# Performance work log

Measured on AMD Instinct MI355X. Metric: run time of the kernel, lower is better.

Reference implementation:

```python
import jax, jax.numpy as jnp
import numpy as np

EMBED_DIM = 768
N_HEADS = 12
HEAD_SIZE = EMBED_DIM // N_HEADS
SCALE = HEAD_SIZE ** -0.5


def setup_inputs() -> dict:
    key = jax.random.key(0)
    k1, k2, k3, k4, k5 = jax.random.split(key, 5)
    B, T, C = 2, 4096, EMBED_DIM
    x = jax.random.normal(k1, (B, T, C), dtype=jnp.float32)
    # nn.Linear(embed_dim, 3*embed_dim): weight [3C, C], bias [3C]
    w_attn = jax.random.normal(k2, (3 * C, C), dtype=jnp.float32) * (C ** -0.5)
    b_attn = jax.random.normal(k3, (3 * C,), dtype=jnp.float32) * 0.02
    # nn.Linear(embed_dim, embed_dim)
    w_proj = jax.random.normal(k4, (C, C), dtype=jnp.float32) * (C ** -0.5)
    b_proj = jax.random.normal(k5, (C,), dtype=jnp.float32) * 0.02
    return {"x": x, "w_attn": w_attn, "b_attn": b_attn, "w_proj": w_proj, "b_proj": b_proj}


def reference(x, w_attn, b_attn, w_proj, b_proj):
    b, t, c = x.shape
    qkv = jnp.einsum('btc,dc->btd', x, w_attn) + b_attn  # [b,t,3c]
    q, k, v = jnp.split(qkv, 3, axis=-1)
    # [b, h, t, hs]
    q = q.reshape(b, t, N_HEADS, HEAD_SIZE).transpose(0, 2, 1, 3)
    k = k.reshape(b, t, N_HEADS, HEAD_SIZE).transpose(0, 2, 1, 3)
    v = v.reshape(b, t, N_HEADS, HEAD_SIZE).transpose(0, 2, 1, 3)
    scores = jnp.einsum('bhqd,bhkd->bhqk', q, k) * SCALE  # [b,h,t,t]
    causal = jnp.tril(jnp.ones((t, t), dtype=bool))
    scores = jnp.where(causal[None, None], scores, -jnp.inf)
    attn = jax.nn.softmax(scores, axis=-1)
    out = jnp.einsum('bhqk,bhkd->bhqd', attn, v)  # [b,h,t,hs]
    out = out.transpose(0, 2, 1, 3).reshape(b, t, c)
    out = jnp.einsum('btc,dc->btd', out, w_proj) + b_proj
    return out
```

## Files before the change

kernel.cpp:

```cpp
#include <hip/hip_runtime.h>
#include <hip/hip_bf16.h>

#define T_SEQ 4096
#define C_EMB 768
#define NH_ 12
#define HS_ 64
#define B_SZ 2
#define M_TOK 8192
#define N_QKV 2304

typedef __attribute__((ext_vector_type(8))) __bf16 bf16x8;
typedef __attribute__((ext_vector_type(8))) unsigned short ushort8v;
typedef __attribute__((ext_vector_type(2))) unsigned int uint2v;
typedef __attribute__((ext_vector_type(4))) unsigned int uint4v;
typedef __attribute__((ext_vector_type(4))) float f32x4;

__device__ __forceinline__ unsigned short f2bf(float f) {
  __hip_bfloat16 h = __float2bfloat16(f);
  return __builtin_bit_cast(unsigned short, h);
}

__device__ __forceinline__ unsigned int cvtpk(float lo, float hi) {
  unsigned int r;
  asm("v_cvt_pk_bf16_f32 %0, %1, %2" : "=v"(r) : "v"(lo), "v"(hi));
  return r;
}

__device__ __forceinline__ float fast_exp2(float x) {
  float r;
  asm("v_exp_f32 %0, %1" : "=v"(r) : "v"(x));
  return r;
}

#define GLOAD_LDS16(gp, lp)                                                   \
  __builtin_amdgcn_global_load_lds(                                           \
      (const __attribute__((address_space(1))) void*)(gp),                    \
      (__attribute__((address_space(3))) void*)(lp), 16, 0, 0)

#define KSWZ(row, bytecol) ((((row) * 128) + ((bytecol) ^ (((row) & 7) << 4))))

#define LOG2E 1.4426950408889634f

#define CVT_N0 (M_TOK * C_EMB)
#define CVT_N1 (N_QKV * C_EMB)
#define CVT_N2 (C_EMB * C_EMB)
__global__ void cvt_all_bf16(const float* __restrict__ x,
                             const float* __restrict__ wa,
                             const float* __restrict__ wp,
                             unsigned short* __restrict__ out) {
  int i = (blockIdx.x * 256 + threadIdx.x) * 8;
  const float* src;
  int j;
  if (i < CVT_N0) { src = x; j = i; }
  else if (i < CVT_N0 + CVT_N1) { src = wa; j = i - CVT_N0; }
  else { src = wp; j = i - CVT_N0 - CVT_N1; }
  float4 a = *reinterpret_cast<const float4*>(&src[j]);
  float4 b = *reinterpret_cast<const float4*>(&src[j + 4]);
  uint4v o;
  o.x = cvtpk(a.x, a.y);
  o.y = cvtpk(a.z, a.w);
  o.z = cvtpk(b.x, b.y);
  o.w = cvtpk(b.z, b.w);
  *reinterpret_cast<uint4v*>(&out[i]) = o;
}

template <int MODE, int BM, int BN>
__global__ __launch_bounds__(256) void gemm_bt_kernel(
    const unsigned short* __restrict__ A, const unsigned short* __restrict__ Bw,
    const float* __restrict__ bias, unsigned short* __restrict__ qo,
    unsigned short* __restrict__ ko, unsigned short* __restrict__ vo,
    float* __restrict__ fo, int Kdim, int Ndim) {
  constexpr int MF = BM / 32;
  constexpr int NF = BN / 32;
  __shared__ __align__(16) char as_[BM * 128];
  __shared__ __align__(16) char bs_[BN * 128];
  const int tid = threadIdx.x;
  const int lane = tid & 63;
  const int wid = tid >> 6;
  const int g = lane >> 4;
  const int l15 = lane & 15;
  const int m0 = blockIdx.y * BM;
  const int n0 = blockIdx.x * BN;
  const int wm = (wid >> 1) * (BM / 2);
  const int wn = (wid & 1) * (BN / 2);

  const int lrow = lane >> 3;
  const int scol = ((lane & 7) ^ lrow) * 8;

  f32x4 acc[MF][NF];
#pragma unroll
  for (int i = 0; i < MF; ++i)
#pragma unroll
    for (int j = 0; j < NF; ++j) acc[i][j] = (f32x4){0.f, 0.f, 0.f, 0.f};

  for (int k0 = 0; k0 < Kdim; k0 += 64) {
#pragma unroll
    for (int i = 0; i < BM / 32; ++i) {
      const int r = wid * (BM / 4) + i * 8 + lrow;
      GLOAD_LDS16(&A[(size_t)(m0 + r) * Kdim + k0 + scol],
                  as_ + wid * (BM * 32) + i * 1024);
    }
#pragma unroll
    for (int i = 0; i < BN / 32; ++i) {
      const int r = wid * (BN / 4) + i * 8 + lrow;
      GLOAD_LDS16(&Bw[(size_t)(n0 + r) * Kdim + k0 + scol],
                  bs_ + wid * (BN * 32) + i * 1024);
    }
    __syncthreads();
#pragma unroll
    for (int ks = 0; ks < 2; ++ks) {
      bf16x8 af[MF], bfr[NF];
#pragma unroll
      for (int mf = 0; mf < MF; ++mf) {
        const int ra = wm + mf * 16 + l15;
        af[mf] = __builtin_bit_cast(bf16x8,
            *reinterpret_cast<const ushort8v*>(as_ + KSWZ(ra, ks * 64 + g * 16)));
      }
#pragma unroll
      for (int nf = 0; nf < NF; ++nf) {
        const int rb = wn + nf * 16 + l15;
        bfr[nf] = __builtin_bit_cast(bf16x8,
            *reinterpret_cast<const ushort8v*>(bs_ + KSWZ(rb, ks * 64 + g * 16)));
      }
#pragma unroll
      for (int mf = 0; mf < MF; ++mf)
#pragma unroll
        for (int nf = 0; nf < NF; ++nf)
          acc[mf][nf] = __builtin_amdgcn_mfma_f32_16x16x32_bf16(
              af[mf], bfr[nf], acc[mf][nf], 0, 0, 0);
    }
    __syncthreads();
  }

#pragma unroll
  for (int mf = 0; mf < MF; ++mf)
#pragma unroll
    for (int nf = 0; nf < NF; ++nf) {
      const int n = n0 + wn + nf * 16 + l15;
      const float bval = bias[n];
      float v4[4];
#pragma unroll
      for (int r2 = 0; r2 < 4; ++r2) v4[r2] = acc[mf][nf][r2] + bval;
      const int mb = m0 + wm + mf * 16 + g * 4;
      if (MODE == 1) {
#pragma unroll
        for (int r2 = 0; r2 < 4; ++r2)
          fo[(size_t)(mb + r2) * Ndim + n] = v4[r2];
      } else {
        const int which = (n >= 1536) ? 2 : ((n >= 768) ? 1 : 0);
        const int c = n - which * 768;
        const int h = c >> 6, d = c & 63;
        const int bI = mb >> 12, t = mb & 4095;
        if (which == 0) {
          const size_t off = ((size_t)(bI * NH_ + h) * T_SEQ + t) * HS_ + d;
#pragma unroll
          for (int r2 = 0; r2 < 4; ++r2)
            qo[off + (size_t)r2 * HS_] = f2bf(v4[r2] * 0.125f);
        } else if (which == 1) {
          const size_t off = ((size_t)(bI * NH_ + h) * T_SEQ + t) * HS_ + d;
#pragma unroll
          for (int r2 = 0; r2 < 4; ++r2)
            ko[off + (size_t)r2 * HS_] = f2bf(v4[r2]);
        } else {
          const size_t off = ((size_t)(bI * NH_ + h) * HS_ + d) * T_SEQ + t;
          uint2v o;
          o.x = cvtpk(v4[0], v4[1]);
          o.y = cvtpk(v4[2], v4[3]);
          *reinterpret_cast<uint2v*>(&vo[off]) = o;
        }
      }
    }
}

__global__ __launch_bounds__(256, 3) void flash_kernel(
    const unsigned short* __restrict__ Qg, const unsigned short* __restrict__ Kg,
    const unsigned short* __restrict__ Vtg, unsigned short* __restrict__ Og) {
  __shared__ __align__(16) char ksm[2][8192];
  __shared__ __align__(16) char vtm[2][8192];
  __shared__ __align__(16) char pls[16384];
  const int tid = threadIdx.x;
  const int lane = tid & 63;
  const int wid = tid >> 6;
  const int g = lane >> 4;
  const int l15 = lane & 15;

  const int cc = blockIdx.x & 255, kk = blockIdx.x >> 8;
  const int m = (kk == 0) ? (767 - cc) : ((kk == 1) ? (256 + cc) : cc);
  const int qt = m / 24;
  const int bh = m - qt * 24;
  const int q0 = qt * 128;
  const int b_ = bh / NH_, h_ = bh % NH_;
  const size_t kqbase = (size_t)bh * T_SEQ * HS_;
  const size_t vtbase = (size_t)bh * HS_ * T_SEQ;
  const int wq0 = wid * 32;

  bf16x8 qf[2][2];
#pragma unroll
  for (int nf = 0; nf < 2; ++nf)
#pragma unroll
    for (int ks = 0; ks < 2; ++ks)
      qf[nf][ks] = __builtin_bit_cast(bf16x8,
          *reinterpret_cast<const ushort8v*>(
              &Qg[kqbase + (size_t)(q0 + wq0 + nf * 16 + l15) * HS_ + ks * 32 + g * 8]));

  ushort8v ou;
#pragma unroll
  for (int j = 0; j < 8; ++j) ou[j] = 0x3f80;
  const bf16x8 ones_f = __builtin_bit_cast(bf16x8, ou);

  float m_run[2] = {-1e30f, -1e30f};
  float ml2[2] = {-1.4427e30f, -1.4427e30f};
  f32x4 oacc[2][4];
  f32x4 lacc[2];
#pragma unroll
  for (int nf = 0; nf < 2; ++nf) {
    lacc[nf] = (f32x4){0.f, 0.f, 0.f, 0.f};
#pragma unroll
    for (int j = 0; j < 4; ++j) oacc[nf][j] = (f32x4){0.f, 0.f, 0.f, 0.f};
  }

  char* pw = pls + wid * 4096;

  const int nkt = 2 * qt + 2;
  const int myt = ((q0 + wq0 + 31) >> 6) + 1;

  int sr[2], sc[2];
  const unsigned short* kgp[2];
  const unsigned short* vgp[2];
#pragma unroll
  for (int it = 0; it < 2; ++it) {
    int ci = tid + it * 256;
    sr[it] = ci >> 3;
    sc[it] = (ci & 7) * 16;
    kgp[it] = &Kg[kqbase + (size_t)sr[it] * HS_ + (sc[it] >> 1)];
    vgp[it] = &Vtg[vtbase + (size_t)sr[it] * T_SEQ + (sc[it] >> 1)];
  }

  ushort8v kreg[2], vreg[2];
#pragma unroll
  for (int it = 0; it < 2; ++it) {
    kreg[it] = *reinterpret_cast<const ushort8v*>(kgp[it]);
    vreg[it] = *reinterpret_cast<const ushort8v*>(vgp[it]);
  }
#pragma unroll
  for (int it = 0; it < 2; ++it) {
    *reinterpret_cast<ushort8v*>(&ksm[0][KSWZ(sr[it], sc[it])]) = kreg[it];
    *reinterpret_cast<ushort8v*>(&vtm[0][KSWZ(sr[it], sc[it])]) = vreg[it];
  }
  if (nkt > 1) {
#pragma unroll
    for (int it = 0; it < 2; ++it) {
      kreg[it] = *reinterpret_cast<const ushort8v*>(kgp[it] + (size_t)64 * HS_);
      vreg[it] = *reinterpret_cast<const ushort8v*>(vgp[it] + 64);
    }
  }

  for (int kt = 0; kt < nkt; ++kt) {
    __syncthreads();
    const int cur = kt & 1;
    if (kt + 1 < nkt) {
#pragma unroll
      for (int it = 0; it < 2; ++it) {
        *reinterpret_cast<ushort8v*>(&ksm[cur ^ 1][KSWZ(sr[it], sc[it])]) = kreg[it];
        *reinterpret_cast<ushort8v*>(&vtm[cur ^ 1][KSWZ(sr[it], sc[it])]) = vreg[it];
      }
      if (kt + 2 < nkt) {
        const int k2 = (kt + 2) << 6;
#pragma unroll
        for (int it = 0; it < 2; ++it) {
          kreg[it] = *reinterpret_cast<const ushort8v*>(kgp[it] + (size_t)k2 * HS_);
          vreg[it] = *reinterpret_cast<const ushort8v*>(vgp[it] + k2);
        }
      }
    }

    if (kt < myt) {
      const int k0 = kt << 6;
      const char* kb = ksm[cur];
      const char* vb = vtm[cur];

      f32x4 st[4][2];
#pragma unroll
      for (int i = 0; i < 4; ++i)
#pragma unroll
        for (int j = 0; j < 2; ++j) st[i][j] = (f32x4){0.f, 0.f, 0.f, 0.f};
#pragma unroll
      for (int ks = 0; ks < 2; ++ks) {
        bf16x8 kf[4];
#pragma unroll
        for (int mf = 0; mf < 4; ++mf)
          kf[mf] = __builtin_bit_cast(bf16x8,
              *reinterpret_cast<const ushort8v*>(
                  kb + KSWZ(mf * 16 + l15, ks * 64 + g * 16)));
#pragma unroll
        for (int mf = 0; mf < 4; ++mf)
#pragma unroll
          for (int nf = 0; nf < 2; ++nf)
            st[mf][nf] = __builtin_amdgcn_mfma_f32_16x16x32_bf16(
                kf[mf], qf[nf][ks], st[mf][nf], 0, 0, 0);
      }

      if (k0 + 63 > q0 + wq0) {
#pragma unroll
        for (int mf = 0; mf < 4; ++mf)
#pragma unroll
          for (int nf = 0; nf < 2; ++nf) {
            const int tq = q0 + wq0 + nf * 16 + l15;
#pragma unroll
            for (int r2 = 0; r2 < 4; ++r2) {
              const int tk = k0 + mf * 16 + g * 4 + r2;
              if (tk > tq) st[mf][nf][r2] = -1e30f;
            }
          }
      }

      float mx[2];
#pragma unroll
      for (int nf = 0; nf < 2; ++nf) {
        float v = fmaxf(fmaxf(st[0][nf][0], st[0][nf][1]),
                        fmaxf(st[0][nf][2], st[0][nf][3]));
        v = fmaxf(v, fmaxf(fmaxf(st[1][nf][0], st[1][nf][1]),
                           fmaxf(st[1][nf][2], st[1][nf][3])));
        v = fmaxf(v, fmaxf(fmaxf(st[2][nf][0], st[2][nf][1]),
                           fmaxf(st[2][nf][2], st[2][nf][3])));
        v = fmaxf(v, fmaxf(fmaxf(st[3][nf][0], st[3][nf][1]),
                           fmaxf(st[3][nf][2], st[3][nf][3])));
        v = fmaxf(v, __shfl_xor(v, 16));
        v = fmaxf(v, __shfl_xor(v, 32));
        mx[nf] = v;
      }
      if (__any((mx[0] > m_run[0] + 8.f) || (mx[1] > m_run[1] + 8.f))) {
#pragma unroll
        for (int nf = 0; nf < 2; ++nf) {
          const float mnew = fmaxf(m_run[nf], mx[nf]);
          const float alpha = fast_exp2((m_run[nf] - mnew) * LOG2E);
#pragma unroll
          for (int nd = 0; nd < 4; ++nd)
#pragma unroll
            for (int r2 = 0; r2 < 4; ++r2) oacc[nf][nd][r2] *= alpha;
#pragma unroll
          for (int r2 = 0; r2 < 4; ++r2) lacc[nf][r2] *= alpha;
          m_run[nf] = mnew;
          ml2[nf] = mnew * LOG2E;
        }
      }

#pragma unroll
      for (int mf = 0; mf < 4; ++mf)
#pragma unroll
        for (int nf = 0; nf < 2; ++nf) {
          const float p0 = fast_exp2(fmaf(st[mf][nf][0], LOG2E, -ml2[nf]));
          const float p1 = fast_exp2(fmaf(st[mf][nf][1], LOG2E, -ml2[nf]));
          const float p2 = fast_exp2(fmaf(st[mf][nf][2], LOG2E, -ml2[nf]));
          const float p3 = fast_exp2(fmaf(st[mf][nf][3], LOG2E, -ml2[nf]));
          uint2v w;
          w.x = cvtpk(p0, p1);
          w.y = cvtpk(p2, p3);
          *reinterpret_cast<uint2v*>(
              pw + KSWZ(nf * 16 + l15, mf * 32 + g * 8)) = w;
        }

#pragma unroll
      for (int ks = 0; ks < 2; ++ks) {
        bf16x8 pf[2];
#pragma unroll
        for (int nf = 0; nf < 2; ++nf)
          pf[nf] = __builtin_bit_cast(bf16x8,
              *reinterpret_cast<const ushort8v*>(
                  pw + KSWZ(nf * 16 + l15, ks * 64 + g * 16)));
        bf16x8 vt[4];
#pragma unroll
        for (int nd = 0; nd < 4; ++nd)
          vt[nd] = __builtin_bit_cast(bf16x8,
              *reinterpret_cast<const ushort8v*>(
                  vb + KSWZ(nd * 16 + l15, ks * 64 + g * 16)));
#pragma unroll
        for (int nf = 0; nf < 2; ++nf) {
#pragma unroll
          for (int nd = 0; nd < 4; ++nd)
            oacc[nf][nd] = __builtin_amdgcn_mfma_f32_16x16x32_bf16(
                vt[nd], pf[nf], oacc[nf][nd], 0, 0, 0);
          lacc[nf] = __builtin_amdgcn_mfma_f32_16x16x32_bf16(
              ones_f, pf[nf], lacc[nf], 0, 0, 0);
        }
      }
    }
  }

#pragma unroll
  for (int nf = 0; nf < 2; ++nf) {
    const float invl = 1.f / lacc[nf][0];
    const int t = q0 + wq0 + nf * 16 + l15;
#pragma unroll
    for (int nd = 0; nd < 4; ++nd) {
      uint2v o;
      o.x = cvtpk(oacc[nf][nd][0] * invl, oacc[nf][nd][1] * invl);
      o.y = cvtpk(oacc[nf][nd][2] * invl, oacc[nf][nd][3] * invl);
      *reinterpret_cast<uint2v*>(
          &Og[((size_t)(b_ * T_SEQ + t)) * C_EMB + h_ * 64 + nd * 16 + g * 4]) = o;
    }
  }
}

extern "C" void kernel_launch(void* const* d_in, const int* in_sizes, int n_in,
                              void* d_out, int out_size, void* d_ws, size_t ws_size,
                              hipStream_t stream) {
  const float* x = (const float*)d_in[0];
  const float* w_attn = (const float*)d_in[1];
  const float* b_attn = (const float*)d_in[2];
  const float* w_proj = (const float*)d_in[3];
  const float* b_proj = (const float*)d_in[4];
  float* out = (float*)d_out;

  char* ws = (char*)d_ws;
  size_t off = 0;
  auto carve = [&](size_t bytes) -> void* {
    void* p = ws + off;
    off += (bytes + 255) & ~(size_t)255;
    return p;
  };
  unsigned short* xbf = (unsigned short*)carve((size_t)M_TOK * C_EMB * 2);
  unsigned short* wab = (unsigned short*)carve((size_t)N_QKV * C_EMB * 2);
  unsigned short* wpb = (unsigned short*)carve((size_t)C_EMB * C_EMB * 2);
  unsigned short* Qb = (unsigned short*)carve((size_t)B_SZ * NH_ * T_SEQ * HS_ * 2);
  unsigned short* Kb = (unsigned short*)carve((size_t)B_SZ * NH_ * T_SEQ * HS_ * 2);
  unsigned short* Vtb = (unsigned short*)carve((size_t)B_SZ * NH_ * T_SEQ * HS_ * 2);
  unsigned short* Ob = (unsigned short*)carve((size_t)M_TOK * C_EMB * 2);

  cvt_all_bf16<<<4224, 256, 0, stream>>>(x, w_attn, w_proj, xbf);

  gemm_bt_kernel<0, 128, 128><<<dim3(N_QKV / 128, M_TOK / 128), 256, 0, stream>>>(
      xbf, wab, b_attn, Qb, Kb, Vtb, nullptr, C_EMB, N_QKV);

  flash_kernel<<<dim3(768), 256, 0, stream>>>(Qb, Kb, Vtb, Ob);

  gemm_bt_kernel<1, 64, 128><<<dim3(C_EMB / 128, M_TOK / 64), 256, 0, stream>>>(
      Ob, wpb, b_proj, nullptr, nullptr, nullptr, out, C_EMB, C_EMB);
}
```

Measured before the change: 152.9 us.

## Split causal flash attention across KV chunks with a separate combine kernel

```diff
diff --git a/kernel.cpp b/kernel.cpp
--- a/kernel.cpp
+++ b/kernel.cpp
@@ -8,6 +8,7 @@
 #define B_SZ 2
 #define M_TOK 8192
 #define N_QKV 2304
+#define NPART 1920
 
 typedef __attribute__((ext_vector_type(8))) __bf16 bf16x8;
 typedef __attribute__((ext_vector_type(8))) unsigned short ushort8v;
@@ -30,6 +31,11 @@
   float r;
   asm("v_exp_f32 %0, %1" : "=v"(r) : "v"(x));
   return r;
+}
+
+__device__ __forceinline__ float bf2f(unsigned short u) {
+  unsigned int v = ((unsigned int)u) << 16;
+  return __builtin_bit_cast(float, v);
 }
 
 #define GLOAD_LDS16(gp, lp)                                                   \
@@ -174,7 +180,8 @@
 
 __global__ __launch_bounds__(256, 3) void flash_kernel(
     const unsigned short* __restrict__ Qg, const unsigned short* __restrict__ Kg,
-    const unsigned short* __restrict__ Vtg, unsigned short* __restrict__ Og) {
+    const unsigned short* __restrict__ Vtg, unsigned short* __restrict__ Pp,
+    float2* __restrict__ Ps) {
   __shared__ __align__(16) char ksm[2][8192];
   __shared__ __align__(16) char vtm[2][8192];
   __shared__ __align__(16) char pls[16384];
@@ -184,12 +191,17 @@
   const int g = lane >> 4;
   const int l15 = lane & 15;
 
-  const int cc = blockIdx.x & 255, kk = blockIdx.x >> 8;
-  const int m = (kk == 0) ? (767 - cc) : ((kk == 1) ? (256 + cc) : cc);
-  const int qt = m / 24;
-  const int bh = m - qt * 24;
+  const int rem = blockIdx.x / 24, bh = blockIdx.x % 24;
+  int qt, w;
+  if (rem < 32)      { qt = 31 - (rem >> 2); w = rem & 3; }
+  else if (rem < 56) { int r = rem - 32; qt = 23 - r / 3; w = r % 3; }
+  else if (rem < 72) { int r = rem - 56; qt = 15 - (r >> 1); w = r & 1; }
+  else               { qt = 7 - (rem - 72); w = 0; }
+  const int kq = qt >> 3;
+  const int pbase = 8 * (kq * (kq + 1) / 2) + (qt - 8 * kq) * (kq + 1);
+  const int p = (pbase + w) * 24 + bh;
+
   const int q0 = qt * 128;
-  const int b_ = bh / NH_, h_ = bh % NH_;
   const size_t kqbase = (size_t)bh * T_SEQ * HS_;
   const size_t vtbase = (size_t)bh * HS_ * T_SEQ;
   const int wq0 = wid * 32;
@@ -222,6 +234,8 @@
   char* pw = pls + wid * 4096;
 
   const int nkt = 2 * qt + 2;
+  const int wstart = w * 16;
+  const int wend = (wstart + 16 < nkt) ? wstart + 16 : nkt;
   const int myt = ((q0 + wq0 + 31) >> 6) + 1;
 
   int sr[2], sc[2];
@@ -239,32 +253,32 @@
   ushort8v kreg[2], vreg[2];
 #pragma unroll
   for (int it = 0; it < 2; ++it) {
-    kreg[it] = *reinterpret_cast<const ushort8v*>(kgp[it]);
-    vreg[it] = *reinterpret_cast<const ushort8v*>(vgp[it]);
+    kreg[it] = *reinterpret_cast<const ushort8v*>(kgp[it] + (size_t)(wstart * 64) * HS_);
+    vreg[it] = *reinterpret_cast<const ushort8v*>(vgp[it] + wstart * 64);
   }
 #pragma unroll
   for (int it = 0; it < 2; ++it) {
     *reinterpret_cast<ushort8v*>(&ksm[0][KSWZ(sr[it], sc[it])]) = kreg[it];
     *reinterpret_cast<ushort8v*>(&vtm[0][KSWZ(sr[it], sc[it])]) = vreg[it];
   }
-  if (nkt > 1) {
+  if (wstart + 1 < wend) {
 #pragma unroll
     for (int it = 0; it < 2; ++it) {
-      kreg[it] = *reinterpret_cast<const ushort8v*>(kgp[it] + (size_t)64 * HS_);
-      vreg[it] = *reinterpret_cast<const ushort8v*>(vgp[it] + 64);
-    }
-  }
-
-  for (int kt = 0; kt < nkt; ++kt) {
+      kreg[it] = *reinterpret_cast<const ushort8v*>(kgp[it] + (size_t)((wstart + 1) * 64) * HS_);
+      vreg[it] = *reinterpret_cast<const ushort8v*>(vgp[it] + (wstart + 1) * 64);
+    }
+  }
+
+  for (int kt = wstart; kt < wend; ++kt) {
     __syncthreads();
-    const int cur = kt & 1;
-    if (kt + 1 < nkt) {
+    const int cur = (kt - wstart) & 1;
+    if (kt + 1 < wend) {
 #pragma unroll
       for (int it = 0; it < 2; ++it) {
         *reinterpret_cast<ushort8v*>(&ksm[cur ^ 1][KSWZ(sr[it], sc[it])]) = kreg[it];
         *reinterpret_cast<ushort8v*>(&vtm[cur ^ 1][KSWZ(sr[it], sc[it])]) = vreg[it];
       }
-      if (kt + 2 < nkt) {
+      if (kt + 2 < wend) {
         const int k2 = (kt + 2) << 6;
 #pragma unroll
         for (int it = 0; it < 2; ++it) {
@@ -353,11 +367,11 @@
           const float p1 = fast_exp2(fmaf(st[mf][nf][1], LOG2E, -ml2[nf]));
           const float p2 = fast_exp2(fmaf(st[mf][nf][2], LOG2E, -ml2[nf]));
           const float p3 = fast_exp2(fmaf(st[mf][nf][3], LOG2E, -ml2[nf]));
-          uint2v w;
-          w.x = cvtpk(p0, p1);
-          w.y = cvtpk(p2, p3);
+          uint2v wv;
+          wv.x = cvtpk(p0, p1);
+          wv.y = cvtpk(p2, p3);
           *reinterpret_cast<uint2v*>(
-              pw + KSWZ(nf * 16 + l15, mf * 32 + g * 8)) = w;
+              pw + KSWZ(nf * 16 + l15, mf * 32 + g * 8)) = wv;
         }
 
 #pragma unroll
@@ -387,18 +401,71 @@
     }
   }
 
+  unsigned short* po = Pp + (size_t)p * 8192;
 #pragma unroll
   for (int nf = 0; nf < 2; ++nf) {
-    const float invl = 1.f / lacc[nf][0];
-    const int t = q0 + wq0 + nf * 16 + l15;
+    const int tql = wq0 + nf * 16 + l15;
+    if (g == 0) Ps[p * 128 + tql] = make_float2(m_run[nf], lacc[nf][0]);
 #pragma unroll
     for (int nd = 0; nd < 4; ++nd) {
       uint2v o;
-      o.x = cvtpk(oacc[nf][nd][0] * invl, oacc[nf][nd][1] * invl);
-      o.y = cvtpk(oacc[nf][nd][2] * invl, oacc[nf][nd][3] * invl);
-      *reinterpret_cast<uint2v*>(
-          &Og[((size_t)(b_ * T_SEQ + t)) * C_EMB + h_ * 64 + nd * 16 + g * 4]) = o;
-    }
+      o.x = cvtpk(oacc[nf][nd][0], oacc[nf][nd][1]);
+      o.y = cvtpk(oacc[nf][nd][2], oacc[nf][nd][3]);
+      *reinterpret_cast<uint2v*>(&po[tql * 64 + nd * 16 + g * 4]) = o;
+    }
+  }
+}
+
+__global__ __launch_bounds__(256) void combine_kernel(
+    const unsigned short* __restrict__ Pp, const float2* __restrict__ Ps,
+    unsigned short* __restrict__ Og) {
+  const int qt = blockIdx.x, bh = blockIdx.y;
+  const int kq = qt >> 3;
+  const int Wn = kq + 1;
+  const int pbase = 8 * (kq * (kq + 1) / 2) + (qt - 8 * kq) * (kq + 1);
+  const int b_ = bh / NH_, h_ = bh % NH_;
+  const int tid = threadIdx.x;
+
+  __shared__ float scl[4][128];
+  if (tid < 128) {
+    float mw[4], lw[4];
+    float mM = -1e30f;
+    for (int w = 0; w < Wn; ++w) {
+      float2 s = Ps[((pbase + w) * 24 + bh) * 128 + tid];
+      mw[w] = s.x; lw[w] = s.y;
+      mM = fmaxf(mM, s.x);
+    }
+    float den = 0.f, ew[4];
+    for (int w = 0; w < Wn; ++w) {
+      ew[w] = fast_exp2((mw[w] - mM) * LOG2E);
+      den += ew[w] * lw[w];
+    }
+    const float inv = 1.f / den;
+    for (int w = 0; w < Wn; ++w) scl[w][tid] = ew[w] * inv;
+  }
+  __syncthreads();
+
+#pragma unroll
+  for (int i = 0; i < 4; ++i) {
+    const int e8 = (i * 256 + tid) * 8;
+    const int t = e8 >> 6, d0 = e8 & 63;
+    float acc[8];
+#pragma unroll
+    for (int j = 0; j < 8; ++j) acc[j] = 0.f;
+    for (int w = 0; w < Wn; ++w) {
+      const float s = scl[w][t];
+      ushort8v v = *reinterpret_cast<const ushort8v*>(
+          &Pp[(size_t)((pbase + w) * 24 + bh) * 8192 + e8]);
+#pragma unroll
+      for (int j = 0; j < 8; ++j) acc[j] = fmaf(s, bf2f(v[j]), acc[j]);
+    }
+    uint4v o;
+    o.x = cvtpk(acc[0], acc[1]);
+    o.y = cvtpk(acc[2], acc[3]);
+    o.z = cvtpk(acc[4], acc[5]);
+    o.w = cvtpk(acc[6], acc[7]);
+    *reinterpret_cast<uint4v*>(
+        &Og[((size_t)(b_ * T_SEQ + qt * 128 + t)) * C_EMB + h_ * 64 + d0]) = o;
   }
 }
 
@@ -426,13 +493,17 @@
   unsigned short* Kb = (unsigned short*)carve((size_t)B_SZ * NH_ * T_SEQ * HS_ * 2);
   unsigned short* Vtb = (unsigned short*)carve((size_t)B_SZ * NH_ * T_SEQ * HS_ * 2);
   unsigned short* Ob = (unsigned short*)carve((size_t)M_TOK * C_EMB * 2);
+  unsigned short* Pp = (unsigned short*)carve((size_t)NPART * 8192 * 2);
+  float2* Ps = (float2*)carve((size_t)NPART * 128 * sizeof(float2));
 
   cvt_all_bf16<<<4224, 256, 0, stream>>>(x, w_attn, w_proj, xbf);
 
   gemm_bt_kernel<0, 128, 128><<<dim3(N_QKV / 128, M_TOK / 128), 256, 0, stream>>>(
       xbf, wab, b_attn, Qb, Kb, Vtb, nullptr, C_EMB, N_QKV);
 
-  flash_kernel<<<dim3(768), 256, 0, stream>>>(Qb, Kb, Vtb, Ob);
+  flash_kernel<<<dim3(NPART), 256, 0, stream>>>(Qb, Kb, Vtb, Pp, Ps);
+
+  combine_kernel<<<dim3(32, 24), 256, 0, stream>>>(Pp, Ps, Ob);
 
   gemm_bt_kernel<1, 64, 128><<<dim3(C_EMB / 128, M_TOK / 64), 256, 0, stream>>>(
       Ob, wpb, b_proj, nullptr, nullptr, nullptr, out, C_EMB, C_EMB);
```

Result: slower. 171.3 us (+12.0%).
